# Performance work log

Hardware: AMD Instinct MI355X
Metric: run time of the kernel (lower is better)

The kernel has to match this reference:

```python
import math
import jax, jax.numpy as jnp
import numpy as np

BH, S, DK = 64, 1024, 64   # batch*heads, seq_len, head dim
FG, FL = 32, 32            # global / local enrichment feature dims
H, B = 16, 4               # mask layout [heads, batch, seq]


def setup_inputs() -> dict:
    key = jax.random.key(0)
    k1, k2, k3, k4, k5, k6 = jax.random.split(key, 6)
    return {
        "query": jax.random.normal(k1, (BH, S, DK), dtype=jnp.float32),
        "key": jax.random.normal(k2, (BH, S, DK), dtype=jnp.float32),
        "value": jax.random.normal(k3, (BH, S, DK), dtype=jnp.float32),
        "local_f": jax.random.normal(k4, (BH, S, FL), dtype=jnp.float32),
        "global_f": jax.random.normal(k5, (BH, S, FG), dtype=jnp.float32),
        "mask": jax.random.randint(k6, (H, B, S), 0, 2, dtype=jnp.int32),
    }


def reference(query, key, value, local_f, global_f, mask):
    dk = query.shape[-1]
    # enrich q/k with global then local features (matches torch concat order)
    pq = jnp.concatenate([query, global_f, local_f], axis=2)   # [BH, S, dk+fg+fl]
    pk = jnp.concatenate([key, global_f, local_f], axis=2)
    scores = jnp.einsum("bqd,bkd->bqk", pq, pk) / math.sqrt(dk)  # [BH, S, S]
    # mask [H, B, S] -> [H*B, S] -> broadcast over query positions
    m = mask.reshape(-1, mask.shape[-1])[:, None, :]            # [H*B, 1, S]
    scores = jnp.where(m == 1, jnp.float32(-1e9), scores)
    attn = jax.nn.softmax(scores, axis=-1)
    return jnp.einsum("bqk,bkd->bqd", attn, value)              # [BH, S, dk]
```

## Files before the change

kernel.cpp:

```cpp
#include <hip/hip_runtime.h>
#include <hip/hip_bf16.h>


#define BHn 64
#define Sn  1024
#define NT  16
#define TILESZ 26624
#define KIMG   18432
#define OSTR 68

typedef __attribute__((ext_vector_type(8)))  __bf16 bf16x8;
typedef __attribute__((ext_vector_type(16))) float  f32x16;
typedef __attribute__((ext_vector_type(4)))  unsigned int u32x4;

__device__ __forceinline__ unsigned f2bf1(float a){
    union { float f; unsigned u; } c; c.f = a;
    return (c.u + 0x7fffu + ((c.u >> 16) & 1u)) >> 16;
}
__device__ __forceinline__ unsigned f2bf2(float a, float b){
    return f2bf1(a) | (f2bf1(b) << 16);
}
__device__ __forceinline__ unsigned pkbf(float a, float b){
    return __builtin_amdgcn_perm(__builtin_bit_cast(unsigned, b),
                                 __builtin_bit_cast(unsigned, a), 0x07060302u);
}

__global__ __launch_bounds__(256)
void attn_prep(const float* __restrict__ K, const float* __restrict__ V,
               const float* __restrict__ LF, const float* __restrict__ GF,
               const int* __restrict__ M, unsigned short* __restrict__ P)
{
    __shared__ __align__(16) unsigned char plds[TILESZ];

    const int tid = threadIdx.x;
    const int bh = blockIdx.x >> 4, ti = blockIdx.x & 15, kb = ti*64;

    #pragma unroll
    for (int i=0;i<2;i++){
        int idx = tid + 256*i, row = idx>>3, c = idx&7;
        const float* s = K + ((size_t)bh*Sn + kb + row)*64 + c*8;
        float4 f0 = *(const float4*)s, f1 = *(const float4*)(s+4);
        u32x4 w; w[0]=f2bf2(f0.x,f0.y); w[1]=f2bf2(f0.z,f0.w);
        w[2]=f2bf2(f1.x,f1.y); w[3]=f2bf2(f1.z,f1.w);
        int kp = row>>5, l31 = row&31, dc = c>>1, h = c&1;
        *(u32x4*)(plds + ((kp*9+dc)*2+h)*512 + l31*16) = w;
    }
    {
        int row = tid>>2, c2 = tid&3;
        const float* s = GF + ((size_t)bh*Sn + kb + row)*32 + c2*8;
        float4 f0 = *(const float4*)s, f1 = *(const float4*)(s+4);
        u32x4 w; w[0]=f2bf2(f0.x,f0.y); w[1]=f2bf2(f0.z,f0.w);
        w[2]=f2bf2(f1.x,f1.y); w[3]=f2bf2(f1.z,f1.w);
        int kp = row>>5, l31 = row&31, dc = 4+(c2>>1), h = c2&1;
        *(u32x4*)(plds + ((kp*9+dc)*2+h)*512 + l31*16) = w;
    }
    {
        int row = tid>>2, c2 = tid&3;
        const float* s = LF + ((size_t)bh*Sn + kb + row)*32 + c2*8;
        float4 f0 = *(const float4*)s, f1 = *(const float4*)(s+4);
        u32x4 w; w[0]=f2bf2(f0.x,f0.y); w[1]=f2bf2(f0.z,f0.w);
        w[2]=f2bf2(f1.x,f1.y); w[3]=f2bf2(f1.z,f1.w);
        int kp = row>>5, l31 = row&31, dc = 6+(c2>>1), h = c2&1;
        *(u32x4*)(plds + ((kp*9+dc)*2+h)*512 + l31*16) = w;
    }
    if (tid < 64){
        int mv = M[(size_t)bh*Sn + kb + tid];
        int kp = tid>>5, l31 = tid&31;
        u32x4 w; w[0] = (mv == 1) ? 0x0000ceacu : 0u;
        w[1]=0u; w[2]=0u; w[3]=0u;
        *(u32x4*)(plds + ((kp*9+8)*2+0)*512 + l31*16) = w;
        u32x4 z; z[0]=0u; z[1]=0u; z[2]=0u; z[3]=0u;
        *(u32x4*)(plds + ((kp*9+8)*2+1)*512 + l31*16) = z;
    }
    {
        int d = tid & 63, g = tid >> 6;
        const float* vb = V + ((size_t)bh*Sn + kb + 16*g)*64 + d;
        const int pm[16] = {0,1,2,3, 8,9,10,11, 4,5,6,7, 12,13,14,15};
        unsigned w[8];
        #pragma unroll
        for (int m=0;m<8;m++)
            w[m] = f2bf2(vb[(size_t)pm[2*m]*64], vb[(size_t)pm[2*m+1]*64]);
        u32x4 a, b;
        a[0]=w[0]; a[1]=w[1]; a[2]=w[2]; a[3]=w[3];
        b[0]=w[4]; b[1]=w[5]; b[2]=w[6]; b[3]=w[7];
        int kp = g>>1, j = g&1, dt = d>>5, l31 = d&31;
        unsigned char* vs = plds + KIMG + (((kp*2+dt)*2+j)*2)*512 + l31*16;
        *(u32x4*)(vs)       = a;
        *(u32x4*)(vs + 512) = b;
    }
    __syncthreads();

    unsigned char* dP = (unsigned char*)P + (size_t)(bh*NT + ti)*TILESZ;
    #pragma unroll
    for (int i=0;i<6;i++){
        int off = tid*16 + i*4096;
        *(u32x4*)(dP + off) = *(const u32x4*)(plds + off);
    }
    {
        int off = tid*16 + 6*4096;
        if (off < TILESZ) *(u32x4*)(dP + off) = *(const u32x4*)(plds + off);
    }
}

__global__ __launch_bounds__(512, 4)
void attn_main(const float* __restrict__ Q, const unsigned short* __restrict__ P,
               const float* __restrict__ GF, const float* __restrict__ LF,
               float* __restrict__ O)
{
    __shared__ __align__(16) unsigned char smem[128*OSTR*4 + 512];
    const int tid  = threadIdx.x;
    const int wave = tid >> 6, lane = tid & 63;
    const int l31  = lane & 31, h = lane >> 5;
    const int qh   = wave >> 1;
    const int kp   = wave & 1;
    const int bh = blockIdx.x & 63;
    const int qb = blockIdx.x >> 6;
    const float SCL = 0.18033688011112042f;

    const int qrow = qb*128 + qh*32 + l31;
    u32x4 qf[9];
    #pragma unroll
    for (int dc = 0; dc < 8; dc++){
        const int cb = dc*16 + 8*h;
        const float* src;
        if (cb < 64)      src = Q  + ((size_t)bh*Sn + qrow)*64 + cb;
        else if (cb < 96) src = GF + ((size_t)bh*Sn + qrow)*32 + (cb - 64);
        else              src = LF + ((size_t)bh*Sn + qrow)*32 + (cb - 96);
        float4 f0 = *(const float4*)src;
        float4 f1 = *(const float4*)(src + 4);
        qf[dc][0] = f2bf2(f0.x*SCL, f0.y*SCL);
        qf[dc][1] = f2bf2(f0.z*SCL, f0.w*SCL);
        qf[dc][2] = f2bf2(f1.x*SCL, f1.y*SCL);
        qf[dc][3] = f2bf2(f1.z*SCL, f1.w*SCL);
    }
    qf[8][0] = h ? 0u : 0x00003f80u;
    qf[8][1] = 0u; qf[8][2] = 0u; qf[8][3] = 0u;

    f32x16 oacc[2];
    #pragma unroll
    for (int dt=0; dt<2; dt++)
        #pragma unroll
        for (int r=0; r<16; r++) oacc[dt][r] = 0.f;
    float lrun = 0.f;

    const unsigned char* kptr = (const unsigned char*)P
        + (size_t)bh*NT*TILESZ + kp*9216 + lane*16;
    const unsigned char* vptr = (const unsigned char*)P
        + (size_t)bh*NT*TILESZ + KIMG + kp*4096 + lane*16;

    for (int t = 0; t < NT; t++){
        const unsigned char* kt = kptr + (size_t)t*TILESZ;
        const unsigned char* vt = vptr + (size_t)t*TILESZ;

        f32x16 acc;
        #pragma unroll
        for (int r=0;r<16;r++) acc[r] = 0.f;
        __builtin_amdgcn_s_setprio(1);
        #pragma unroll
        for (int dc=0; dc<9; dc++){
            u32x4 ar = *(const u32x4*)(kt + dc*1024);
            acc = __builtin_amdgcn_mfma_f32_32x32x16_bf16(
                    __builtin_bit_cast(bf16x8, ar),
                    __builtin_bit_cast(bf16x8, qf[dc]), acc, 0, 0, 0);
        }
        __builtin_amdgcn_s_setprio(0);

        u32x4 va00 = *(const u32x4*)(vt);
        u32x4 va01 = *(const u32x4*)(vt + 1024);
        u32x4 va10 = *(const u32x4*)(vt + 2048);
        u32x4 va11 = *(const u32x4*)(vt + 3072);

        float p[16];
        #pragma unroll
        for (int r=0;r<16;r++) p[r] = __builtin_amdgcn_exp2f(acc[r]);
        float s4[8];
        #pragma unroll
        for (int r=0;r<8;r++) s4[r] = p[2*r] + p[2*r+1];
        #pragma unroll
        for (int r=0;r<4;r++) s4[r] = s4[2*r] + s4[2*r+1];
        lrun += (s4[0]+s4[1]) + (s4[2]+s4[3]);

        unsigned pk[8];
        #pragma unroll
        for (int i=0;i<8;i++) pk[i] = pkbf(p[2*i], p[2*i+1]);
        u32x4 b0, b1;
        b0[0]=pk[0]; b0[1]=pk[1]; b0[2]=pk[2]; b0[3]=pk[3];
        b1[0]=pk[4]; b1[1]=pk[5]; b1[2]=pk[6]; b1[3]=pk[7];

        __builtin_amdgcn_s_setprio(1);
        oacc[0] = __builtin_amdgcn_mfma_f32_32x32x16_bf16(
                __builtin_bit_cast(bf16x8, va00),
                __builtin_bit_cast(bf16x8, b0), oacc[0], 0, 0, 0);
        oacc[0] = __builtin_amdgcn_mfma_f32_32x32x16_bf16(
                __builtin_bit_cast(bf16x8, va01),
                __builtin_bit_cast(bf16x8, b1), oacc[0], 0, 0, 0);
        oacc[1] = __builtin_amdgcn_mfma_f32_32x32x16_bf16(
                __builtin_bit_cast(bf16x8, va10),
                __builtin_bit_cast(bf16x8, b0), oacc[1], 0, 0, 0);
        oacc[1] = __builtin_amdgcn_mfma_f32_32x32x16_bf16(
                __builtin_bit_cast(bf16x8, va11),
                __builtin_bit_cast(bf16x8, b1), oacc[1], 0, 0, 0);
        __builtin_amdgcn_s_setprio(0);
    }

    __syncthreads();
    float lw = lrun + __shfl_xor(lrun, 32, 64);
    float* s1 = (float*)smem;
    float* s2 = (float*)(smem + 128*OSTR*4);
    if (kp == 1){
        #pragma unroll
        for (int dt=0;dt<2;dt++)
            #pragma unroll
            for (int rg=0;rg<4;rg++){
                float4 w;
                w.x = oacc[dt][rg*4+0]; w.y = oacc[dt][rg*4+1];
                w.z = oacc[dt][rg*4+2]; w.w = oacc[dt][rg*4+3];
                *(float4*)(s1 + (qh*32 + l31)*OSTR + dt*32 + rg*8 + 4*h) = w;
            }
        if (h == 0) s2[qh*32 + l31] = lw;
    }
    __syncthreads();
    if (kp == 0){
        float inv = 1.0f / (lw + s2[qh*32 + l31]);
        #pragma unroll
        for (int dt=0;dt<2;dt++)
            #pragma unroll
            for (int rg=0;rg<4;rg++){
                float* p = s1 + (qh*32 + l31)*OSTR + dt*32 + rg*8 + 4*h;
                float4 w = *(float4*)p;
                w.x = (w.x + oacc[dt][rg*4+0])*inv;
                w.y = (w.y + oacc[dt][rg*4+1])*inv;
                w.z = (w.z + oacc[dt][rg*4+2])*inv;
                w.w = (w.w + oacc[dt][rg*4+3])*inv;
                *(float4*)p = w;
            }
    }
    __syncthreads();
    #pragma unroll
    for (int i=0;i<4;i++){
        int idx = tid + 512*i, r = idx>>4, c = idx&15;
        *(float4*)(O + ((size_t)bh*Sn + qb*128 + r)*64 + c*4) =
            *(const float4*)(s1 + r*OSTR + c*4);
    }
}

extern "C" void kernel_launch(void* const* d_in, const int* in_sizes, int n_in,
                              void* d_out, int out_size, void* d_ws, size_t ws_size,
                              hipStream_t stream) {
    const float* Q  = (const float*)d_in[0];
    const float* K  = (const float*)d_in[1];
    const float* V  = (const float*)d_in[2];
    const float* LF = (const float*)d_in[3];
    const float* GF = (const float*)d_in[4];
    const int*   M  = (const int*)d_in[5];
    float* O = (float*)d_out;

    unsigned short* P = (unsigned short*)d_ws;

    attn_prep<<<dim3(BHn*NT), dim3(256), 0, stream>>>(K, V, LF, GF, M, P);
    attn_main<<<dim3(BHn*(Sn/128)), dim3(512), 0, stream>>>(Q, P, GF, LF, O);
}
```

Before: 146.5 us.

## Double-buffer K/V fragment loads in registers across tiles in attention loop

New measurement: 147.4 us. No clear change (+0.6%).

```diff
diff --git a/kernel.cpp b/kernel.cpp
--- a/kernel.cpp
+++ b/kernel.cpp
@@ -102,7 +102,64 @@
     }
 }
 
-__global__ __launch_bounds__(512, 4)
+__device__ __forceinline__ void load_frags(u32x4 (&f)[13],
+                                           const unsigned char* kt,
+                                           const unsigned char* vt){
+    #pragma unroll
+    for (int i=0;i<9;i++) f[i] = *(const u32x4*)(kt + i*1024);
+    #pragma unroll
+    for (int i=0;i<4;i++) f[9+i] = *(const u32x4*)(vt + i*1024);
+}
+
+__device__ __forceinline__ void tile_compute(const u32x4 (&f)[13],
+                                             const u32x4 (&qf)[9],
+                                             f32x16& o0, f32x16& o1,
+                                             float& lrun){
+    f32x16 acc;
+    #pragma unroll
+    for (int r=0;r<16;r++) acc[r] = 0.f;
+    __builtin_amdgcn_s_setprio(1);
+    #pragma unroll
+    for (int dc=0; dc<9; dc++)
+        acc = __builtin_amdgcn_mfma_f32_32x32x16_bf16(
+                __builtin_bit_cast(bf16x8, f[dc]),
+                __builtin_bit_cast(bf16x8, qf[dc]), acc, 0, 0, 0);
+    __builtin_amdgcn_s_setprio(0);
+
+    float p[16];
+    #pragma unroll
+    for (int r=0;r<16;r++) p[r] = __builtin_amdgcn_exp2f(acc[r]);
+    float s4[8];
+    #pragma unroll
+    for (int r=0;r<8;r++) s4[r] = p[2*r] + p[2*r+1];
+    #pragma unroll
+    for (int r=0;r<4;r++) s4[r] = s4[2*r] + s4[2*r+1];
+    lrun += (s4[0]+s4[1]) + (s4[2]+s4[3]);
+
+    unsigned pk[8];
+    #pragma unroll
+    for (int i=0;i<8;i++) pk[i] = pkbf(p[2*i], p[2*i+1]);
+    u32x4 b0, b1;
+    b0[0]=pk[0]; b0[1]=pk[1]; b0[2]=pk[2]; b0[3]=pk[3];
+    b1[0]=pk[4]; b1[1]=pk[5]; b1[2]=pk[6]; b1[3]=pk[7];
+
+    __builtin_amdgcn_s_setprio(1);
+    o0 = __builtin_amdgcn_mfma_f32_32x32x16_bf16(
+            __builtin_bit_cast(bf16x8, f[9]),
+            __builtin_bit_cast(bf16x8, b0), o0, 0, 0, 0);
+    o0 = __builtin_amdgcn_mfma_f32_32x32x16_bf16(
+            __builtin_bit_cast(bf16x8, f[10]),
+            __builtin_bit_cast(bf16x8, b1), o0, 0, 0, 0);
+    o1 = __builtin_amdgcn_mfma_f32_32x32x16_bf16(
+            __builtin_bit_cast(bf16x8, f[11]),
+            __builtin_bit_cast(bf16x8, b0), o1, 0, 0, 0);
+    o1 = __builtin_amdgcn_mfma_f32_32x32x16_bf16(
+            __builtin_bit_cast(bf16x8, f[12]),
+            __builtin_bit_cast(bf16x8, b1), o1, 0, 0, 0);
+    __builtin_amdgcn_s_setprio(0);
+}
+
+__global__ __launch_bounds__(512, 2)
 void attn_main(const float* __restrict__ Q, const unsigned short* __restrict__ P,
                const float* __restrict__ GF, const float* __restrict__ LF,
                float* __restrict__ O)
@@ -117,6 +174,14 @@
     const int qb = blockIdx.x >> 6;
     const float SCL = 0.18033688011112042f;
 
+    const unsigned char* kptr = (const unsigned char*)P
+        + (size_t)bh*NT*TILESZ + kp*9216 + lane*16;
+    const unsigned char* vptr = (const unsigned char*)P
+        + (size_t)bh*NT*TILESZ + KIMG + kp*4096 + lane*16;
+
+    u32x4 fA[13], fB[13];
+    load_frags(fA, kptr, vptr);
+
     const int qrow = qb*128 + qh*32 + l31;
     u32x4 qf[9];
     #pragma unroll
@@ -136,71 +201,17 @@
     qf[8][0] = h ? 0u : 0x00003f80u;
     qf[8][1] = 0u; qf[8][2] = 0u; qf[8][3] = 0u;
 
-    f32x16 oacc[2];
-    #pragma unroll
-    for (int dt=0; dt<2; dt++)
-        #pragma unroll
-        for (int r=0; r<16; r++) oacc[dt][r] = 0.f;
+    f32x16 oacc0, oacc1;
+    #pragma unroll
+    for (int r=0; r<16; r++){ oacc0[r] = 0.f; oacc1[r] = 0.f; }
     float lrun = 0.f;
 
-    const unsigned char* kptr = (const unsigned char*)P
-        + (size_t)bh*NT*TILESZ + kp*9216 + lane*16;
-    const unsigned char* vptr = (const unsigned char*)P
-        + (size_t)bh*NT*TILESZ + KIMG + kp*4096 + lane*16;
-
-    for (int t = 0; t < NT; t++){
-        const unsigned char* kt = kptr + (size_t)t*TILESZ;
-        const unsigned char* vt = vptr + (size_t)t*TILESZ;
-
-        f32x16 acc;
-        #pragma unroll
-        for (int r=0;r<16;r++) acc[r] = 0.f;
-        __builtin_amdgcn_s_setprio(1);
-        #pragma unroll
-        for (int dc=0; dc<9; dc++){
-            u32x4 ar = *(const u32x4*)(kt + dc*1024);
-            acc = __builtin_amdgcn_mfma_f32_32x32x16_bf16(
-                    __builtin_bit_cast(bf16x8, ar),
-                    __builtin_bit_cast(bf16x8, qf[dc]), acc, 0, 0, 0);
-        }
-        __builtin_amdgcn_s_setprio(0);
-
-        u32x4 va00 = *(const u32x4*)(vt);
-        u32x4 va01 = *(const u32x4*)(vt + 1024);
-        u32x4 va10 = *(const u32x4*)(vt + 2048);
-        u32x4 va11 = *(const u32x4*)(vt + 3072);
-
-        float p[16];
-        #pragma unroll
-        for (int r=0;r<16;r++) p[r] = __builtin_amdgcn_exp2f(acc[r]);
-        float s4[8];
-        #pragma unroll
-        for (int r=0;r<8;r++) s4[r] = p[2*r] + p[2*r+1];
-        #pragma unroll
-        for (int r=0;r<4;r++) s4[r] = s4[2*r] + s4[2*r+1];
-        lrun += (s4[0]+s4[1]) + (s4[2]+s4[3]);
-
-        unsigned pk[8];
-        #pragma unroll
-        for (int i=0;i<8;i++) pk[i] = pkbf(p[2*i], p[2*i+1]);
-        u32x4 b0, b1;
-        b0[0]=pk[0]; b0[1]=pk[1]; b0[2]=pk[2]; b0[3]=pk[3];
-        b1[0]=pk[4]; b1[1]=pk[5]; b1[2]=pk[6]; b1[3]=pk[7];
-
-        __builtin_amdgcn_s_setprio(1);
-        oacc[0] = __builtin_amdgcn_mfma_f32_32x32x16_bf16(
-                __builtin_bit_cast(bf16x8, va00),
-                __builtin_bit_cast(bf16x8, b0), oacc[0], 0, 0, 0);
-        oacc[0] = __builtin_amdgcn_mfma_f32_32x32x16_bf16(
-                __builtin_bit_cast(bf16x8, va01),
-                __builtin_bit_cast(bf16x8, b1), oacc[0], 0, 0, 0);
-        oacc[1] = __builtin_amdgcn_mfma_f32_32x32x16_bf16(
-                __builtin_bit_cast(bf16x8, va10),
-                __builtin_bit_cast(bf16x8, b0), oacc[1], 0, 0, 0);
-        oacc[1] = __builtin_amdgcn_mfma_f32_32x32x16_bf16(
-                __builtin_bit_cast(bf16x8, va11),
-                __builtin_bit_cast(bf16x8, b1), oacc[1], 0, 0, 0);
-        __builtin_amdgcn_s_setprio(0);
+    for (int tp = 0; tp < NT; tp += 2){
+        load_frags(fB, kptr + (size_t)(tp+1)*TILESZ, vptr + (size_t)(tp+1)*TILESZ);
+        tile_compute(fA, qf, oacc0, oacc1, lrun);
+        if (tp+2 < NT)
+            load_frags(fA, kptr + (size_t)(tp+2)*TILESZ, vptr + (size_t)(tp+2)*TILESZ);
+        tile_compute(fB, qf, oacc0, oacc1, lrun);
     }
 
     __syncthreads();
@@ -209,31 +220,38 @@
     float* s2 = (float*)(smem + 128*OSTR*4);
     if (kp == 1){
         #pragma unroll
-        for (int dt=0;dt<2;dt++)
-            #pragma unroll
-            for (int rg=0;rg<4;rg++){
-                float4 w;
-                w.x = oacc[dt][rg*4+0]; w.y = oacc[dt][rg*4+1];
-                w.z = oacc[dt][rg*4+2]; w.w = oacc[dt][rg*4+3];
-                *(float4*)(s1 + (qh*32 + l31)*OSTR + dt*32 + rg*8 + 4*h) = w;
-            }
+        for (int rg=0;rg<4;rg++){
+            float4 w;
+            w.x = oacc0[rg*4+0]; w.y = oacc0[rg*4+1];
+            w.z = oacc0[rg*4+2]; w.w = oacc0[rg*4+3];
+            *(float4*)(s1 + (qh*32 + l31)*OSTR + rg*8 + 4*h) = w;
+            float4 v;
+            v.x = oacc1[rg*4+0]; v.y = oacc1[rg*4+1];
+            v.z = oacc1[rg*4+2]; v.w = oacc1[rg*4+3];
+            *(float4*)(s1 + (qh*32 + l31)*OSTR + 32 + rg*8 + 4*h) = v;
+        }
         if (h == 0) s2[qh*32 + l31] = lw;
     }
     __syncthreads();
     if (kp == 0){
         float inv = 1.0f / (lw + s2[qh*32 + l31]);
         #pragma unroll
-        for (int dt=0;dt<2;dt++)
-            #pragma unroll
-            for (int rg=0;rg<4;rg++){
-                float* p = s1 + (qh*32 + l31)*OSTR + dt*32 + rg*8 + 4*h;
-                float4 w = *(float4*)p;
-                w.x = (w.x + oacc[dt][rg*4+0])*inv;
-                w.y = (w.y + oacc[dt][rg*4+1])*inv;
-                w.z = (w.z + oacc[dt][rg*4+2])*inv;
-                w.w = (w.w + oacc[dt][rg*4+3])*inv;
-                *(float4*)p = w;
-            }
+        for (int rg=0;rg<4;rg++){
+            float* p = s1 + (qh*32 + l31)*OSTR + rg*8 + 4*h;
+            float4 w = *(float4*)p;
+            w.x = (w.x + oacc0[rg*4+0])*inv;
+            w.y = (w.y + oacc0[rg*4+1])*inv;
+            w.z = (w.z + oacc0[rg*4+2])*inv;
+            w.w = (w.w + oacc0[rg*4+3])*inv;
+            *(float4*)p = w;
+            float* q = s1 + (qh*32 + l31)*OSTR + 32 + rg*8 + 4*h;
+            float4 v = *(float4*)q;
+            v.x = (v.x + oacc1[rg*4+0])*inv;
+            v.y = (v.y + oacc1[rg*4+1])*inv;
+            v.z = (v.z + oacc1[rg*4+2])*inv;
+            v.w = (v.w + oacc1[rg*4+3])*inv;
+            *(float4*)q = v;
+        }
     }
     __syncthreads();
     #pragma unroll
```

## Double-buffer K/V tiles in LDS via async global-to-LDS loads

Applied to the files above, without the earlier changes.

Measured after the change: 139.5 us. -4.8%, faster.

```diff
diff --git a/kernel.cpp b/kernel.cpp
--- a/kernel.cpp
+++ b/kernel.cpp
@@ -8,6 +8,7 @@
 #define TILESZ 26624
 #define KIMG   18432
 #define OSTR 68
+#define WAIT_VM0 0x0F70
 
 typedef __attribute__((ext_vector_type(8)))  __bf16 bf16x8;
 typedef __attribute__((ext_vector_type(16))) float  f32x16;
@@ -23,6 +24,11 @@
 __device__ __forceinline__ unsigned pkbf(float a, float b){
     return __builtin_amdgcn_perm(__builtin_bit_cast(unsigned, b),
                                  __builtin_bit_cast(unsigned, a), 0x07060302u);
+}
+__device__ __forceinline__ void gld_lds16(const void* g, void* l){
+    __builtin_amdgcn_global_load_lds(
+        (const __attribute__((address_space(1))) unsigned int*)g,
+        (__attribute__((address_space(3))) unsigned int*)l, 16, 0, 0);
 }
 
 __global__ __launch_bounds__(256)
@@ -107,7 +113,7 @@
                const float* __restrict__ GF, const float* __restrict__ LF,
                float* __restrict__ O)
 {
-    __shared__ __align__(16) unsigned char smem[128*OSTR*4 + 512];
+    __shared__ __align__(16) unsigned char smem[2*TILESZ];
     const int tid  = threadIdx.x;
     const int wave = tid >> 6, lane = tid & 63;
     const int l31  = lane & 31, h = lane >> 5;
@@ -143,14 +149,29 @@
         for (int r=0; r<16; r++) oacc[dt][r] = 0.f;
     float lrun = 0.f;
 
-    const unsigned char* kptr = (const unsigned char*)P
-        + (size_t)bh*NT*TILESZ + kp*9216 + lane*16;
-    const unsigned char* vptr = (const unsigned char*)P
-        + (size_t)bh*NT*TILESZ + KIMG + kp*4096 + lane*16;
+    const unsigned char* gTb = (const unsigned char*)P + (size_t)bh*NT*TILESZ;
+
+    #pragma unroll
+    for (int i=0;i<4;i++){
+        int c = wave + 8*i;
+        if (c < 26) gld_lds16(gTb + (size_t)c*1024 + lane*16, smem + c*1024);
+    }
+    __builtin_amdgcn_s_waitcnt(WAIT_VM0);
 
     for (int t = 0; t < NT; t++){
-        const unsigned char* kt = kptr + (size_t)t*TILESZ;
-        const unsigned char* vt = vptr + (size_t)t*TILESZ;
+        unsigned char* cur = smem + (size_t)(t&1)*TILESZ;
+        unsigned char* nxt = smem + (size_t)((t+1)&1)*TILESZ;
+        __syncthreads();
+        if (t+1 < NT){
+            const unsigned char* gT = gTb + (size_t)(t+1)*TILESZ;
+            #pragma unroll
+            for (int i=0;i<4;i++){
+                int c = wave + 8*i;
+                if (c < 26) gld_lds16(gT + (size_t)c*1024 + lane*16, nxt + c*1024);
+            }
+        }
+        const unsigned char* kt = cur + kp*9216 + lane*16;
+        const unsigned char* vt = cur + KIMG + kp*4096 + lane*16;
 
         f32x16 acc;
         #pragma unroll
@@ -165,11 +186,6 @@
         }
         __builtin_amdgcn_s_setprio(0);
 
-        u32x4 va00 = *(const u32x4*)(vt);
-        u32x4 va01 = *(const u32x4*)(vt + 1024);
-        u32x4 va10 = *(const u32x4*)(vt + 2048);
-        u32x4 va11 = *(const u32x4*)(vt + 3072);
-
         float p[16];
         #pragma unroll
         for (int r=0;r<16;r++) p[r] = __builtin_amdgcn_exp2f(acc[r]);
@@ -188,19 +204,20 @@
         b1[0]=pk[4]; b1[1]=pk[5]; b1[2]=pk[6]; b1[3]=pk[7];
 
         __builtin_amdgcn_s_setprio(1);
-        oacc[0] = __builtin_amdgcn_mfma_f32_32x32x16_bf16(
-                __builtin_bit_cast(bf16x8, va00),
-                __builtin_bit_cast(bf16x8, b0), oacc[0], 0, 0, 0);
-        oacc[0] = __builtin_amdgcn_mfma_f32_32x32x16_bf16(
-                __builtin_bit_cast(bf16x8, va01),
-                __builtin_bit_cast(bf16x8, b1), oacc[0], 0, 0, 0);
-        oacc[1] = __builtin_amdgcn_mfma_f32_32x32x16_bf16(
-                __builtin_bit_cast(bf16x8, va10),
-                __builtin_bit_cast(bf16x8, b0), oacc[1], 0, 0, 0);
-        oacc[1] = __builtin_amdgcn_mfma_f32_32x32x16_bf16(
-                __builtin_bit_cast(bf16x8, va11),
-                __builtin_bit_cast(bf16x8, b1), oacc[1], 0, 0, 0);
+        #pragma unroll
+        for (int dt=0;dt<2;dt++){
+            u32x4 va0 = *(const u32x4*)(vt + dt*2048);
+            u32x4 va1 = *(const u32x4*)(vt + dt*2048 + 1024);
+            oacc[dt] = __builtin_amdgcn_mfma_f32_32x32x16_bf16(
+                    __builtin_bit_cast(bf16x8, va0),
+                    __builtin_bit_cast(bf16x8, b0), oacc[dt], 0, 0, 0);
+            oacc[dt] = __builtin_amdgcn_mfma_f32_32x32x16_bf16(
+                    __builtin_bit_cast(bf16x8, va1),
+                    __builtin_bit_cast(bf16x8, b1), oacc[dt], 0, 0, 0);
+        }
         __builtin_amdgcn_s_setprio(0);
+
+        __builtin_amdgcn_s_waitcnt(WAIT_VM0);
     }
 
     __syncthreads();
```

## Stage K/V tiles into LDS via async global_load_lds double buffering and bitmask masking

Applied to the files above, without the earlier changes.

Result: faster. 140.6 us (-4.0%).

```diff
diff --git a/kernel.cpp b/kernel.cpp
--- a/kernel.cpp
+++ b/kernel.cpp
@@ -5,9 +5,10 @@
 #define BHn 64
 #define Sn  1024
 #define NT  16
-#define TILESZ 26624
-#define KIMG   18432
+#define TILESZ 24576
+#define KIMG2  16384
 #define OSTR 68
+#define WAIT_VM0 0x0F70
 
 typedef __attribute__((ext_vector_type(8)))  __bf16 bf16x8;
 typedef __attribute__((ext_vector_type(16))) float  f32x16;
@@ -24,11 +25,17 @@
     return __builtin_amdgcn_perm(__builtin_bit_cast(unsigned, b),
                                  __builtin_bit_cast(unsigned, a), 0x07060302u);
 }
+__device__ __forceinline__ void gld_lds16(const void* g, void* l){
+    __builtin_amdgcn_global_load_lds(
+        (const __attribute__((address_space(1))) unsigned int*)g,
+        (__attribute__((address_space(3))) unsigned int*)l, 16, 0, 0);
+}
 
 __global__ __launch_bounds__(256)
 void attn_prep(const float* __restrict__ K, const float* __restrict__ V,
                const float* __restrict__ LF, const float* __restrict__ GF,
-               const int* __restrict__ M, unsigned short* __restrict__ P)
+               const int* __restrict__ M, unsigned short* __restrict__ P,
+               unsigned long long* __restrict__ Mb)
 {
     __shared__ __align__(16) unsigned char plds[TILESZ];
 
@@ -43,7 +50,7 @@
         u32x4 w; w[0]=f2bf2(f0.x,f0.y); w[1]=f2bf2(f0.z,f0.w);
         w[2]=f2bf2(f1.x,f1.y); w[3]=f2bf2(f1.z,f1.w);
         int kp = row>>5, l31 = row&31, dc = c>>1, h = c&1;
-        *(u32x4*)(plds + ((kp*9+dc)*2+h)*512 + l31*16) = w;
+        *(u32x4*)(plds + ((kp*8+dc)*2+h)*512 + l31*16) = w;
     }
     {
         int row = tid>>2, c2 = tid&3;
@@ -52,7 +59,7 @@
         u32x4 w; w[0]=f2bf2(f0.x,f0.y); w[1]=f2bf2(f0.z,f0.w);
         w[2]=f2bf2(f1.x,f1.y); w[3]=f2bf2(f1.z,f1.w);
         int kp = row>>5, l31 = row&31, dc = 4+(c2>>1), h = c2&1;
-        *(u32x4*)(plds + ((kp*9+dc)*2+h)*512 + l31*16) = w;
+        *(u32x4*)(plds + ((kp*8+dc)*2+h)*512 + l31*16) = w;
     }
     {
         int row = tid>>2, c2 = tid&3;
@@ -61,16 +68,12 @@
         u32x4 w; w[0]=f2bf2(f0.x,f0.y); w[1]=f2bf2(f0.z,f0.w);
         w[2]=f2bf2(f1.x,f1.y); w[3]=f2bf2(f1.z,f1.w);
         int kp = row>>5, l31 = row&31, dc = 6+(c2>>1), h = c2&1;
-        *(u32x4*)(plds + ((kp*9+dc)*2+h)*512 + l31*16) = w;
+        *(u32x4*)(plds + ((kp*8+dc)*2+h)*512 + l31*16) = w;
     }
     if (tid < 64){
         int mv = M[(size_t)bh*Sn + kb + tid];
-        int kp = tid>>5, l31 = tid&31;
-        u32x4 w; w[0] = (mv == 1) ? 0x0000ceacu : 0u;
-        w[1]=0u; w[2]=0u; w[3]=0u;
-        *(u32x4*)(plds + ((kp*9+8)*2+0)*512 + l31*16) = w;
-        u32x4 z; z[0]=0u; z[1]=0u; z[2]=0u; z[3]=0u;
-        *(u32x4*)(plds + ((kp*9+8)*2+1)*512 + l31*16) = z;
+        unsigned long long bal = __ballot(mv == 1);
+        if (tid == 0) Mb[bh*NT + ti] = bal;
     }
     {
         int d = tid & 63, g = tid >> 6;
@@ -84,7 +87,7 @@
         a[0]=w[0]; a[1]=w[1]; a[2]=w[2]; a[3]=w[3];
         b[0]=w[4]; b[1]=w[5]; b[2]=w[6]; b[3]=w[7];
         int kp = g>>1, j = g&1, dt = d>>5, l31 = d&31;
-        unsigned char* vs = plds + KIMG + (((kp*2+dt)*2+j)*2)*512 + l31*16;
+        unsigned char* vs = plds + KIMG2 + (((kp*2+dt)*2+j)*2)*512 + l31*16;
         *(u32x4*)(vs)       = a;
         *(u32x4*)(vs + 512) = b;
     }
@@ -96,18 +99,15 @@
         int off = tid*16 + i*4096;
         *(u32x4*)(dP + off) = *(const u32x4*)(plds + off);
     }
-    {
-        int off = tid*16 + 6*4096;
-        if (off < TILESZ) *(u32x4*)(dP + off) = *(const u32x4*)(plds + off);
-    }
 }
 
 __global__ __launch_bounds__(512, 4)
 void attn_main(const float* __restrict__ Q, const unsigned short* __restrict__ P,
+               const unsigned long long* __restrict__ Mb,
                const float* __restrict__ GF, const float* __restrict__ LF,
                float* __restrict__ O)
 {
-    __shared__ __align__(16) unsigned char smem[128*OSTR*4 + 512];
+    __shared__ __align__(16) unsigned char smem[2*TILESZ];
     const int tid  = threadIdx.x;
     const int wave = tid >> 6, lane = tid & 63;
     const int l31  = lane & 31, h = lane >> 5;
@@ -118,7 +118,7 @@
     const float SCL = 0.18033688011112042f;
 
     const int qrow = qb*128 + qh*32 + l31;
-    u32x4 qf[9];
+    u32x4 qf[8];
     #pragma unroll
     for (int dc = 0; dc < 8; dc++){
         const int cb = dc*16 + 8*h;
@@ -133,8 +133,6 @@
         qf[dc][2] = f2bf2(f1.x*SCL, f1.y*SCL);
         qf[dc][3] = f2bf2(f1.z*SCL, f1.w*SCL);
     }
-    qf[8][0] = h ? 0u : 0x00003f80u;
-    qf[8][1] = 0u; qf[8][2] = 0u; qf[8][3] = 0u;
 
     f32x16 oacc[2];
     #pragma unroll
@@ -143,21 +141,41 @@
         for (int r=0; r<16; r++) oacc[dt][r] = 0.f;
     float lrun = 0.f;
 
-    const unsigned char* kptr = (const unsigned char*)P
-        + (size_t)bh*NT*TILESZ + kp*9216 + lane*16;
-    const unsigned char* vptr = (const unsigned char*)P
-        + (size_t)bh*NT*TILESZ + KIMG + kp*4096 + lane*16;
+    const unsigned char* gTb = (const unsigned char*)P + (size_t)bh*NT*TILESZ;
+
+    #pragma unroll
+    for (int i=0;i<3;i++){
+        int c = wave + 8*i;
+        gld_lds16(gTb + (size_t)c*1024 + lane*16, smem + c*1024);
+    }
+    __builtin_amdgcn_s_waitcnt(WAIT_VM0);
 
     for (int t = 0; t < NT; t++){
-        const unsigned char* kt = kptr + (size_t)t*TILESZ;
-        const unsigned char* vt = vptr + (size_t)t*TILESZ;
+        unsigned char* cur = smem + (size_t)(t&1)*TILESZ;
+        unsigned char* nxt = smem + (size_t)((t+1)&1)*TILESZ;
+        __syncthreads();
+        if (t+1 < NT){
+            const unsigned char* gT = gTb + (size_t)(t+1)*TILESZ;
+            #pragma unroll
+            for (int i=0;i<3;i++){
+                int c = wave + 8*i;
+                gld_lds16(gT + (size_t)c*1024 + lane*16, nxt + c*1024);
+            }
+        }
+        const unsigned char* kt = cur + kp*8192 + lane*16;
+        const unsigned char* vt = cur + KIMG2 + kp*4096 + lane*16;
+
+        u32x4 va00 = *(const u32x4*)(vt);
+        u32x4 va01 = *(const u32x4*)(vt + 1024);
+        u32x4 va10 = *(const u32x4*)(vt + 2048);
+        u32x4 va11 = *(const u32x4*)(vt + 3072);
 
         f32x16 acc;
         #pragma unroll
         for (int r=0;r<16;r++) acc[r] = 0.f;
         __builtin_amdgcn_s_setprio(1);
         #pragma unroll
-        for (int dc=0; dc<9; dc++){
+        for (int dc=0; dc<8; dc++){
             u32x4 ar = *(const u32x4*)(kt + dc*1024);
             acc = __builtin_amdgcn_mfma_f32_32x32x16_bf16(
                     __builtin_bit_cast(bf16x8, ar),
@@ -165,14 +183,17 @@
         }
         __builtin_amdgcn_s_setprio(0);
 
-        u32x4 va00 = *(const u32x4*)(vt);
-        u32x4 va01 = *(const u32x4*)(vt + 1024);
-        u32x4 va10 = *(const u32x4*)(vt + 2048);
-        u32x4 va11 = *(const u32x4*)(vt + 3072);
+        unsigned long long mw = Mb[bh*NT + t];
+        unsigned w32 = kp ? (unsigned)(mw >> 32) : (unsigned)mw;
+        unsigned wsh = w32 >> (4*h);
 
         float p[16];
         #pragma unroll
-        for (int r=0;r<16;r++) p[r] = __builtin_amdgcn_exp2f(acc[r]);
+        for (int r=0;r<16;r++){
+            float pr = __builtin_amdgcn_exp2f(acc[r]);
+            unsigned bit = (wsh >> ((r&3)+8*(r>>2))) & 1u;
+            p[r] = bit ? 0.f : pr;
+        }
         float s4[8];
         #pragma unroll
         for (int r=0;r<8;r++) s4[r] = p[2*r] + p[2*r+1];
@@ -201,6 +222,8 @@
                 __builtin_bit_cast(bf16x8, va11),
                 __builtin_bit_cast(bf16x8, b1), oacc[1], 0, 0, 0);
         __builtin_amdgcn_s_setprio(0);
+
+        __builtin_amdgcn_s_waitcnt(WAIT_VM0);
     }
 
     __syncthreads();
@@ -255,8 +278,9 @@
     const int*   M  = (const int*)d_in[5];
     float* O = (float*)d_out;
 
-    unsigned short* P = (unsigned short*)d_ws;
-
-    attn_prep<<<dim3(BHn*NT), dim3(256), 0, stream>>>(K, V, LF, GF, M, P);
-    attn_main<<<dim3(BHn*(Sn/128)), dim3(512), 0, stream>>>(Q, P, GF, LF, O);
-}
+    unsigned short*     P  = (unsigned short*)d_ws;
+    unsigned long long* Mb = (unsigned long long*)((char*)d_ws + (size_t)BHn*NT*TILESZ);
+
+    attn_prep<<<dim3(BHn*NT), dim3(256), 0, stream>>>(K, V, LF, GF, M, P, Mb);
+    attn_main<<<dim3(BHn*(Sn/128)), dim3(512), 0, stream>>>(Q, P, Mb, GF, LF, O);
+}
```
